# Kernel tuning notes

Measured on AMD Instinct MI355X. Metric: run time of the kernel, lower is better.

## Reference

```python
import jax, jax.numpy as jnp
import numpy as np

N, E, G = 4096, 16384, 16
IN_C, EDGE_C, H = 3, 4, 128
LN_EPS = 1e-5


def setup_inputs() -> dict:
    key = jax.random.key(0)
    ks = jax.random.split(key, 32)
    nrm = lambda k, shp, s: jax.random.normal(k, shp, jnp.float32) * s
    inp = {}
    inp["x"] = nrm(ks[0], (N, IN_C), 1.0)
    inp["edge_index"] = jax.random.randint(ks[1], (2, E), 0, N)
    inp["edge_attr"] = nrm(ks[2], (E, EDGE_C), 1.0)
    inp["batch"] = jnp.sort(jax.random.randint(ks[3], (N,), 0, G))
    inp["contingency_type"] = nrm(ks[4], (G, 4), 1.0)
    inp["load_scale"] = nrm(ks[5], (G,), 1.0)
    i = 6
    def conv_params(prefix, in_c):
        nonlocal i
        inp[prefix + "_w1"] = nrm(ks[i], (EDGE_C, 128), 1.0 / np.sqrt(EDGE_C)); i += 1
        inp[prefix + "_b1"] = jnp.zeros((128,), jnp.float32)
        inp[prefix + "_w2"] = nrm(ks[i], (128, in_c * H), 1.0 / np.sqrt(128)); i += 1
        inp[prefix + "_b2"] = jnp.zeros((in_c * H,), jnp.float32)
        inp[prefix + "_root"] = nrm(ks[i], (in_c, H), 1.0 / np.sqrt(in_c)); i += 1
        inp[prefix + "_bias"] = jnp.zeros((H,), jnp.float32)
    conv_params("c1", IN_C)
    conv_params("c2", H)
    conv_params("c3", H)
    for p in ("ln1", "ln2", "ln3"):
        inp[p + "_g"] = jnp.ones((H,), jnp.float32)
        inp[p + "_b"] = jnp.zeros((H,), jnp.float32)
    inp["lin_w"] = nrm(ks[i], (2 * H + 4 + 1, 2), 1.0 / np.sqrt(2 * H + 5)); i += 1
    inp["lin_b"] = jnp.zeros((2,), jnp.float32)
    return inp


def _nnconv(x, src, dst, edge_attr, w1, b1, w2, b2, root, bias, in_c):
    # edge MLP -> per-edge weight matrix [E, in_c, H]
    h = jax.nn.relu(edge_attr @ w1 + b1)
    W = (h @ w2 + b2).reshape(-1, in_c, H)
    msg = jnp.einsum('ei,eio->eo', x[src], W)  # gather + per-edge matmul
    s = jax.ops.segment_sum(msg, dst, num_segments=N)
    cnt = jax.ops.segment_sum(jnp.ones((msg.shape[0],), msg.dtype), dst, num_segments=N)
    agg = s / jnp.maximum(cnt, 1.0)[:, None]  # scatter-mean
    return agg + x @ root + bias


def _layernorm(x, g, b):
    m = jnp.mean(x, axis=-1, keepdims=True)
    v = jnp.mean(jnp.square(x - m), axis=-1, keepdims=True)
    return (x - m) * jax.lax.rsqrt(v + LN_EPS) * g + b


def reference(x, edge_index, edge_attr, batch, contingency_type, load_scale,
              c1_w1, c1_b1, c1_w2, c1_b2, c1_root, c1_bias,
              c2_w1, c2_b1, c2_w2, c2_b2, c2_root, c2_bias,
              c3_w1, c3_b1, c3_w2, c3_b2, c3_root, c3_bias,
              ln1_g, ln1_b, ln2_g, ln2_b, ln3_g, ln3_b,
              lin_w, lin_b):
    src, dst = edge_index[0], edge_index[1]
    h = _nnconv(x, src, dst, edge_attr, c1_w1, c1_b1, c1_w2, c1_b2, c1_root, c1_bias, IN_C)
    h = jax.nn.relu(_layernorm(h, ln1_g, ln1_b))
    h = _nnconv(h, src, dst, edge_attr, c2_w1, c2_b1, c2_w2, c2_b2, c2_root, c2_bias, H)
    h = jax.nn.elu(_layernorm(h, ln2_g, ln2_b))
    h = _nnconv(h, src, dst, edge_attr, c3_w1, c3_b1, c3_w2, c3_b2, c3_root, c3_bias, H)
    h = jax.nn.leaky_relu(_layernorm(h, ln3_g, ln3_b), negative_slope=0.01)
    # global mean / max pool over graphs
    gsum = jax.ops.segment_sum(h, batch, num_segments=G)
    gcnt = jax.ops.segment_sum(jnp.ones((N,), h.dtype), batch, num_segments=G)
    gmean = gsum / jnp.maximum(gcnt, 1.0)[:, None]
    gmax = jax.ops.segment_max(h, batch, num_segments=G)
    gmax = jnp.where(gcnt[:, None] > 0, gmax, 0.0)
    x_cat = jnp.concatenate([gmean, gmax, contingency_type, load_scale[:, None]], axis=1)
    return x_cat @ lin_w + lin_b
```

## Files before the change

### kernel.cpp

```cpp
#include <hip/hip_runtime.h>
#include <hip/hip_bf16.h>


#define N_NODES 4096
#define N_EDGES 16384
#define N_GRAPHS 16
#define HD 128
#define BM 128
#define LDB 136
#define KSPLIT 2
#define KT_PER (HD / KSPLIT)
#define SLAB_E (HD * HD)
#define PN 32

typedef unsigned short ushort_t;
typedef __attribute__((ext_vector_type(8))) short short8;
typedef __attribute__((ext_vector_type(4))) float f32x4;

static __device__ __forceinline__ ushort_t f2b(float f) {
    __hip_bfloat16 h = __float2bfloat16(f);
    union { __hip_bfloat16 h; ushort_t u; } cv; cv.h = h; return cv.u;
}
static __device__ __forceinline__ float b2f(ushort_t u) {
    union { unsigned u; float f; } cv; cv.u = ((unsigned)u) << 16; return cv.f;
}

static __device__ __forceinline__ float wave_sum(float v) {
#pragma unroll
    for (int off = 1; off < 64; off <<= 1) v += __shfl_xor(v, off, 64);
    return v;
}

__global__ __launch_bounds__(256) void count_k(const int* __restrict__ dst, float* __restrict__ cnt) {
    int e = blockIdx.x * 256 + threadIdx.x;
    atomicAdd(&cnt[dst[e]], 1.0f);
}

__global__ __launch_bounds__(128) void l1_edge(
    const float* __restrict__ x, const int* __restrict__ src, const int* __restrict__ dst,
    const float* __restrict__ ea, const float* __restrict__ w1, const float* __restrict__ b1,
    const float* __restrict__ w2, const float* __restrict__ b2, float* __restrict__ agg) {
    __shared__ float h[4][HD];
    __shared__ float xsrc[4][3];
    const int o = threadIdx.x;
    const int e0 = blockIdx.x * 4;
#pragma unroll
    for (int q = 0; q < 4; ++q) {
        float s = b1[o];
#pragma unroll
        for (int j = 0; j < 4; ++j) s = fmaf(ea[(e0 + q) * 4 + j], w1[j * HD + o], s);
        h[q][o] = fmaxf(s, 0.0f);
    }
    if (o < 12) { int q = o / 3, i = o % 3; xsrc[q][i] = x[src[e0 + q] * 3 + i]; }
    __syncthreads();
    float acc[4] = {0.f, 0.f, 0.f, 0.f};
    for (int i = 0; i < 3; ++i) {
        float bb = b2[i * HD + o];
        float w[4] = {bb, bb, bb, bb};
        for (int k = 0; k < HD; ++k) {
            float w2v = w2[k * 384 + i * HD + o];
#pragma unroll
            for (int q = 0; q < 4; ++q) w[q] = fmaf(h[q][k], w2v, w[q]);
        }
#pragma unroll
        for (int q = 0; q < 4; ++q) acc[q] = fmaf(xsrc[q][i], w[q], acc[q]);
    }
#pragma unroll
    for (int q = 0; q < 4; ++q) atomicAdd(&agg[dst[e0 + q] * HD + o], acc[q]);
}

__global__ __launch_bounds__(128) void node_update_l1(
    float* __restrict__ agg, const float* __restrict__ cnt, const float* __restrict__ x,
    const float* __restrict__ root, const float* __restrict__ bias,
    const float* __restrict__ lng, const float* __restrict__ lnb) {
    const int n = blockIdx.x, o = threadIdx.x;
    float s = bias[o];
#pragma unroll
    for (int i = 0; i < 3; ++i) s = fmaf(x[n * 3 + i], root[i * HD + o], s);
    float v = agg[n * HD + o] / fmaxf(cnt[n], 1.0f) + s;
    __shared__ float red[2];
    float ws = wave_sum(v);
    if ((o & 63) == 0) red[o >> 6] = ws;
    __syncthreads();
    float m = (red[0] + red[1]) * (1.0f / HD);
    float d = v - m;
    float ws2 = wave_sum(d * d);
    __syncthreads();
    if ((o & 63) == 0) red[o >> 6] = ws2;
    __syncthreads();
    float var = (red[0] + red[1]) * (1.0f / HD);
    float y = d * rsqrtf(var + 1e-5f) * lng[o] + lnb[o];
    agg[n * HD + o] = fmaxf(y, 0.0f);
}

__global__ __launch_bounds__(256) void w2t_prep(const float* __restrict__ w2,
                                                const float* __restrict__ b2,
                                                ushort_t* __restrict__ w2t) {
    __shared__ ushort_t tile[HD][LDB];
    const int kt = blockIdx.x;
    const int t = threadIdx.x;
    const float* srcp = (kt < HD) ? (w2 + kt * HD * HD) : b2;
    for (int c = 0; c < 64; ++c) {
        int flat = c * 256 + t;
        int i = flat >> 7, o = flat & 127;
        tile[o][i] = f2b(srcp[i * HD + o]);
    }
    __syncthreads();
    uint4* outp = (uint4*)(w2t + kt * HD * HD);
    for (int c = 0; c < 8; ++c) {
        int f = c * 256 + t;
        int o = f >> 4, i0 = (f & 15) * 8;
        outp[f] = *(const uint4*)&tile[o][i0];
    }
}

__global__ __launch_bounds__(512, 2) void gemm_mfma(
    const float* __restrict__ hprev, const float* __restrict__ ea,
    const float* __restrict__ w1, const float* __restrict__ b1,
    const ushort_t* __restrict__ w2t,
    const int* __restrict__ src, const int* __restrict__ dst,
    float* __restrict__ agg) {
    __shared__ ushort_t Bs[4 * SLAB_E];
    __shared__ ushort_t HeT[KT_PER + 1][BM];

    const int t = threadIdx.x;
    const int wave = t >> 6, lane = t & 63;
    const int quad = lane >> 4, l16 = lane & 15;
    const int mg = wave >> 2;
    const int ng = wave & 3;
    const int eb = blockIdx.x >> 1;
    const int ks = blockIdx.x & 1;
    const int k0 = ks * KT_PER;
    const int e0 = eb * BM;
    const int rbase = mg * 64;
    const int n0 = ng * 32;
    const int nslab = ks ? (KT_PER + 1) : KT_PER;

#define GSLAB(s) (((s) < KT_PER) ? (k0 + (s)) : HD)
#define ASMBAR  { asm volatile("s_waitcnt lgkmcnt(0)" ::: "memory"); \
                  __builtin_amdgcn_s_barrier(); }

#define LOADG(va, vb, vc, vd, kt)                                               \
    {                                                                           \
        const uint4* gp = (const uint4*)(w2t + (size_t)(kt) * SLAB_E);          \
        va = gp[t]; vb = gp[t + 512]; vc = gp[t + 1024]; vd = gp[t + 1536];     \
    }
    const int dr0 = t >> 4;
    const int dswoff = dr0 * HD + (((t & 15) ^ (dr0 & 7)) << 3);
#define DSW(wp, va, vb, vc, vd)                                                 \
    {                                                                           \
        *(uint4*)((wp) + dswoff)         = va;                                  \
        *(uint4*)((wp) + dswoff + 4096)  = vb;                                  \
        *(uint4*)((wp) + dswoff + 8192)  = vc;                                  \
        *(uint4*)((wp) + dswoff + 12288) = vd;                                  \
    }
#define READF(bf, bp)                                                           \
    {                                                                           \
        _Pragma("unroll") for (int ni = 0; ni < 2; ++ni) {                      \
            const int R = n0 + ni * 16 + l16;                                   \
            const ushort_t* rowp = (bp) + R * HD;                               \
            const int r7 = R & 7;                                               \
            _Pragma("unroll") for (int kb = 0; kb < 4; ++kb)                    \
                bf[ni][kb] = *(const short8*)&rowp[((kb * 4 + quad) ^ r7) << 3];\
        }                                                                       \
    }
#define CONSUME(bf, s)                                                          \
    {                                                                           \
        _Pragma("unroll") for (int mi = 0; mi < 4; ++mi) {                      \
            ushort4 hv = *(const ushort4*)&HeT[s][rbase + mi * 16 + quad * 4];  \
            float h0 = b2f(hv.x), h1 = b2f(hv.y), h2 = b2f(hv.z), h3 = b2f(hv.w);\
            _Pragma("unroll") for (int ni = 0; ni < 2; ++ni) {                  \
                f32x4 p = {0.f, 0.f, 0.f, 0.f};                                 \
                _Pragma("unroll") for (int kb = 0; kb < 4; ++kb)                \
                    p = __builtin_amdgcn_mfma_f32_16x16x32_bf16(                \
                        afrag[mi][kb], bf[ni][kb], p, 0, 0, 0);                 \
                acc[mi][ni][0] = fmaf(h0, p[0], acc[mi][ni][0]);                \
                acc[mi][ni][1] = fmaf(h1, p[1], acc[mi][ni][1]);                \
                acc[mi][ni][2] = fmaf(h2, p[2], acc[mi][ni][2]);                \
                acc[mi][ni][3] = fmaf(h3, p[3], acc[mi][ni][3]);                \
            }                                                                   \
        }                                                                       \
    }

    uint4 s0a, s0b, s0c, s0d, s1a, s1b, s1c, s1d;
    LOADG(s0a, s0b, s0c, s0d, GSLAB(0));
    LOADG(s1a, s1b, s1c, s1d, GSLAB(1));

    {
        const int le = t >> 2;
        const int j0 = (t & 3) * 4;
        const int r7 = le & 7;
        const float* rp = hprev + src[e0 + le] * HD + (t & 3) * 32;
        ushort_t* xrow = Bs + 3 * (size_t)SLAB_E + le * HD;
#pragma unroll
        for (int c = 0; c < 4; ++c) {
            float4 va = ((const float4*)rp)[2 * c];
            float4 vb = ((const float4*)rp)[2 * c + 1];
            uint4 pk;
            pk.x = (unsigned)f2b(va.x) | ((unsigned)f2b(va.y) << 16);
            pk.y = (unsigned)f2b(va.z) | ((unsigned)f2b(va.w) << 16);
            pk.z = (unsigned)f2b(vb.x) | ((unsigned)f2b(vb.y) << 16);
            pk.w = (unsigned)f2b(vb.z) | ((unsigned)f2b(vb.w) << 16);
            *(uint4*)&xrow[((j0 + c) ^ r7) << 3] = pk;
        }
    }

    {
        const int e = t & 127;
        const float4 av = ((const float4*)ea)[e0 + e];
        const float a0 = av.x, a1 = av.y, a2 = av.z, a3 = av.w;
        for (int kl = t >> 7; kl < KT_PER; kl += 4) {
            const int kt = k0 + kl;
            float s = b1[kt];
            s = fmaf(a0, w1[0 * HD + kt], s);
            s = fmaf(a1, w1[1 * HD + kt], s);
            s = fmaf(a2, w1[2 * HD + kt], s);
            s = fmaf(a3, w1[3 * HD + kt], s);
            HeT[kl][e] = f2b(fmaxf(s, 0.0f));
        }
        if (ks == 1 && (t >> 7) == 0) HeT[KT_PER][e] = f2b(1.0f);
    }
    ASMBAR;

    short8 afrag[4][4];
    {
        const ushort_t* xp = Bs + 3 * (size_t)SLAB_E;
#pragma unroll
        for (int mi = 0; mi < 4; ++mi) {
            const int R = rbase + mi * 16 + l16;
            const ushort_t* rowp = xp + R * HD;
            const int r7 = R & 7;
#pragma unroll
            for (int kb = 0; kb < 4; ++kb)
                afrag[mi][kb] = *(const short8*)&rowp[((kb * 4 + quad) ^ r7) << 3];
        }
    }

    DSW(Bs, s0a, s0b, s0c, s0d);
    DSW(Bs + SLAB_E, s1a, s1b, s1c, s1d);
    LOADG(s0a, s0b, s0c, s0d, GSLAB(2));
    LOADG(s1a, s1b, s1c, s1d, GSLAB(3));

    f32x4 acc[4][2];
#pragma unroll
    for (int mi = 0; mi < 4; ++mi)
#pragma unroll
        for (int ni = 0; ni < 2; ++ni)
            acc[mi][ni] = (f32x4){0.f, 0.f, 0.f, 0.f};

    ASMBAR;

    short8 bf0[2][4], bf1[2][4];
    for (int s = 0; s < KT_PER; s += 2) {
        ushort_t* bpe = Bs + (size_t)(s & 3) * SLAB_E;
        ushort_t* bpo = Bs + (size_t)((s + 1) & 3) * SLAB_E;
        READF(bf0, bpe);
        CONSUME(bf0, s);
        if (s + 2 < nslab) { ushort_t* wp = Bs + (size_t)((s + 2) & 3) * SLAB_E; DSW(wp, s0a, s0b, s0c, s0d); }
        if (s + 3 < nslab) { ushort_t* wp = Bs + (size_t)((s + 3) & 3) * SLAB_E; DSW(wp, s1a, s1b, s1c, s1d); }
        if (s + 4 < nslab) LOADG(s0a, s0b, s0c, s0d, GSLAB(s + 4));
        if (s + 5 < nslab) LOADG(s1a, s1b, s1c, s1d, GSLAB(s + 5));
        READF(bf1, bpo);
        CONSUME(bf1, s + 1);
        ASMBAR;
    }
    if (nslab > KT_PER) {
        ushort_t* bp = Bs + (size_t)(KT_PER & 3) * SLAB_E;
        READF(bf0, bp);
        CONSUME(bf0, KT_PER);
    }
#undef GSLAB
#undef ASMBAR
#undef LOADG
#undef DSW
#undef READF
#undef CONSUME

#pragma unroll
    for (int mi = 0; mi < 4; ++mi) {
#pragma unroll
        for (int r = 0; r < 4; ++r) {
            const int dn = dst[e0 + rbase + mi * 16 + quad * 4 + r];
#pragma unroll
            for (int ni = 0; ni < 2; ++ni)
                atomicAdd(&agg[dn * HD + n0 + ni * 16 + l16], acc[mi][ni][r]);
        }
    }
}

__global__ __launch_bounds__(128) void node_update(
    float* __restrict__ agg, const float* __restrict__ cnt,
    const float* __restrict__ hprev, const float* __restrict__ root, const float* __restrict__ bias,
    const float* __restrict__ lng, const float* __restrict__ lnb, int act) {
    const int n = blockIdx.x, o = threadIdx.x;
    __shared__ float hr[HD];
    hr[o] = hprev[n * HD + o];
    __syncthreads();
    float s = bias[o];
#pragma unroll 8
    for (int k = 0; k < HD; ++k) s = fmaf(hr[k], root[k * HD + o], s);
    float v = agg[n * HD + o] / fmaxf(cnt[n], 1.0f) + s;
    __shared__ float red[2];
    float ws = wave_sum(v);
    if ((o & 63) == 0) red[o >> 6] = ws;
    __syncthreads();
    float m = (red[0] + red[1]) * (1.0f / HD);
    float d = v - m;
    float ws2 = wave_sum(d * d);
    __syncthreads();
    if ((o & 63) == 0) red[o >> 6] = ws2;
    __syncthreads();
    float var = (red[0] + red[1]) * (1.0f / HD);
    float y = d * rsqrtf(var + 1e-5f) * lng[o] + lnb[o];
    if (act == 1) y = (y > 0.0f) ? y : expm1f(y);
    else y = (y > 0.0f) ? y : 0.01f * y;
    agg[n * HD + o] = y;
}

static __device__ __forceinline__ unsigned fkey(float f) {
    unsigned b = __float_as_uint(f);
    return (b & 0x80000000u) ? ~b : (b | 0x80000000u);
}
__global__ __launch_bounds__(128) void pool_scatter(
    const float* __restrict__ h3, const int* __restrict__ batch,
    float* __restrict__ gsum, unsigned* __restrict__ gmaxk, int* __restrict__ gcnt) {
    const int o = threadIdx.x;
    const int nb = blockIdx.x * PN;
    float sum = 0.0f, mx = -3.0e38f;
    int gcur = batch[nb];
    int run = 0;
    for (int j = 0; j < PN; ++j) {
        const int n = nb + j;
        const int g = batch[n];
        const float v = h3[n * HD + o];
        if (g != gcur) {
            atomicAdd(&gsum[gcur * HD + o], sum);
            atomicMax(&gmaxk[gcur * HD + o], fkey(mx));
            if (o == 0) atomicAdd(&gcnt[gcur], run);
            sum = 0.0f; mx = -3.0e38f; run = 0; gcur = g;
        }
        sum += v; mx = fmaxf(mx, v); ++run;
    }
    atomicAdd(&gsum[gcur * HD + o], sum);
    atomicMax(&gmaxk[gcur * HD + o], fkey(mx));
    if (o == 0) atomicAdd(&gcnt[gcur], run);
}

__global__ __launch_bounds__(128) void pool_head2(
    const float* __restrict__ gsum, const unsigned* __restrict__ gmaxk, const int* __restrict__ gcnt,
    const float* __restrict__ cont, const float* __restrict__ ls,
    const float* __restrict__ lin_w, const float* __restrict__ lin_b, float* __restrict__ out) {
    const int g = blockIdx.x, o = threadIdx.x;
    const int c = gcnt[g];
    __shared__ float xcat[2 * HD + 5];
    xcat[o] = gsum[g * HD + o] / fmaxf((float)c, 1.0f);
    unsigned key = gmaxk[g * HD + o];
    unsigned bits = (key & 0x80000000u) ? (key & 0x7FFFFFFFu) : ~key;
    xcat[HD + o] = (c > 0) ? __uint_as_float(bits) : 0.0f;
    if (o < 4) xcat[2 * HD + o] = cont[g * 4 + o];
    if (o == 0) xcat[2 * HD + 4] = ls[g];
    __syncthreads();
    if (o < 2) {
        float r = lin_b[o];
        for (int ri = 0; ri < 2 * HD + 5; ++ri) r = fmaf(xcat[ri], lin_w[ri * 2 + o], r);
        out[g * 2 + o] = r;
    }
}

extern "C" void kernel_launch(void* const* d_in, const int* in_sizes, int n_in,
                              void* d_out, int out_size, void* d_ws, size_t ws_size,
                              hipStream_t stream) {
    const float* x     = (const float*)d_in[0];
    const int*   ei    = (const int*)d_in[1];
    const float* ea    = (const float*)d_in[2];
    const int*   batch = (const int*)d_in[3];
    const float* cont  = (const float*)d_in[4];
    const float* ls    = (const float*)d_in[5];
    const float *c1_w1 = (const float*)d_in[6],  *c1_b1 = (const float*)d_in[7];
    const float *c1_w2 = (const float*)d_in[8],  *c1_b2 = (const float*)d_in[9];
    const float *c1_rt = (const float*)d_in[10], *c1_bs = (const float*)d_in[11];
    const float *c2_w1 = (const float*)d_in[12], *c2_b1 = (const float*)d_in[13];
    const float *c2_w2 = (const float*)d_in[14], *c2_b2 = (const float*)d_in[15];
    const float *c2_rt = (const float*)d_in[16], *c2_bs = (const float*)d_in[17];
    const float *c3_w1 = (const float*)d_in[18], *c3_b1 = (const float*)d_in[19];
    const float *c3_w2 = (const float*)d_in[20], *c3_b2 = (const float*)d_in[21];
    const float *c3_rt = (const float*)d_in[22], *c3_bs = (const float*)d_in[23];
    const float *ln1g = (const float*)d_in[24], *ln1b = (const float*)d_in[25];
    const float *ln2g = (const float*)d_in[26], *ln2b = (const float*)d_in[27];
    const float *ln3g = (const float*)d_in[28], *ln3b = (const float*)d_in[29];
    const float *lin_w = (const float*)d_in[30], *lin_b = (const float*)d_in[31];
    float* out = (float*)d_out;

    float*    cnt  = (float*)d_ws;
    float*    bufA = cnt + N_NODES;
    float*    bufB = bufA + N_NODES * HD;
    ushort_t* w2t  = (ushort_t*)(bufB + N_NODES * HD);
    float*    gsum = (float*)(w2t + (HD + 1) * HD * HD);
    unsigned* gmaxk = (unsigned*)(gsum + N_GRAPHS * HD);
    int*      gcnt = (int*)(gmaxk + N_GRAPHS * HD);
    const int* src = ei;
    const int* dst = ei + N_EDGES;

    hipMemsetAsync(cnt, 0, N_NODES * sizeof(float), stream);
    count_k<<<N_EDGES / 256, 256, 0, stream>>>(dst, cnt);

    hipMemsetAsync(bufA, 0, N_NODES * HD * sizeof(float), stream);
    l1_edge<<<N_EDGES / 4, 128, 0, stream>>>(x, src, dst, ea, c1_w1, c1_b1, c1_w2, c1_b2, bufA);
    node_update_l1<<<N_NODES, 128, 0, stream>>>(bufA, cnt, x, c1_rt, c1_bs, ln1g, ln1b);

    w2t_prep<<<HD + 1, 256, 0, stream>>>(c2_w2, c2_b2, w2t);
    hipMemsetAsync(bufB, 0, N_NODES * HD * sizeof(float), stream);
    gemm_mfma<<<(N_EDGES / BM) * KSPLIT, 512, 0, stream>>>(bufA, ea, c2_w1, c2_b1, w2t, src, dst, bufB);
    node_update<<<N_NODES, 128, 0, stream>>>(bufB, cnt, bufA, c2_rt, c2_bs, ln2g, ln2b, 1);

    w2t_prep<<<HD + 1, 256, 0, stream>>>(c3_w2, c3_b2, w2t);
    hipMemsetAsync(bufA, 0, N_NODES * HD * sizeof(float), stream);
    gemm_mfma<<<(N_EDGES / BM) * KSPLIT, 512, 0, stream>>>(bufB, ea, c3_w1, c3_b1, w2t, src, dst, bufA);
    node_update<<<N_NODES, 128, 0, stream>>>(bufA, cnt, bufB, c3_rt, c3_bs, ln3g, ln3b, 2);

    hipMemsetAsync(gsum, 0, (2 * N_GRAPHS * HD + N_GRAPHS) * sizeof(float), stream);
    pool_scatter<<<N_NODES / PN, 128, 0, stream>>>(bufA, batch, gsum, gmaxk, gcnt);
    pool_head2<<<N_GRAPHS, 128, 0, stream>>>(gsum, gmaxk, gcnt, cont, ls, lin_w, lin_b, out);
}
```

Before: 388.0 us.

## Split K four ways and double-buffer weight slabs to raise occupancy

Splits the per-edge hidden dimension across four blocks instead of two, so more blocks run per edge tile. The shared weight buffer shrinks from four slabs to two, with a reworked double-buffered load/store schedule, and launch bounds now target four blocks per CU. The bias slab is handled by a separate consume path that adds the product directly, replacing the multiply by a constant row of ones. In exchange, every edge tile is gathered and converted four times instead of twice, atomic adds to the aggregate double, and the tighter pipeline has less prefetch depth.

```diff
diff --git a/kernel.cpp b/kernel.cpp
--- a/kernel.cpp
+++ b/kernel.cpp
@@ -8,7 +8,7 @@
 #define HD 128
 #define BM 128
 #define LDB 136
-#define KSPLIT 2
+#define KSPLIT 4
 #define KT_PER (HD / KSPLIT)
 #define SLAB_E (HD * HD)
 #define PN 32
@@ -114,27 +114,27 @@
     }
 }
 
-__global__ __launch_bounds__(512, 2) void gemm_mfma(
+__global__ __launch_bounds__(512, 4) void gemm_mfma(
     const float* __restrict__ hprev, const float* __restrict__ ea,
     const float* __restrict__ w1, const float* __restrict__ b1,
     const ushort_t* __restrict__ w2t,
     const int* __restrict__ src, const int* __restrict__ dst,
     float* __restrict__ agg) {
-    __shared__ ushort_t Bs[4 * SLAB_E];
-    __shared__ ushort_t HeT[KT_PER + 1][BM];
+    __shared__ ushort_t Bs[2 * SLAB_E];
+    __shared__ ushort_t HeT[KT_PER][BM];
 
     const int t = threadIdx.x;
     const int wave = t >> 6, lane = t & 63;
     const int quad = lane >> 4, l16 = lane & 15;
     const int mg = wave >> 2;
     const int ng = wave & 3;
-    const int eb = blockIdx.x >> 1;
-    const int ks = blockIdx.x & 1;
+    const int eb = blockIdx.x >> 2;
+    const int ks = blockIdx.x & 3;
     const int k0 = ks * KT_PER;
     const int e0 = eb * BM;
     const int rbase = mg * 64;
     const int n0 = ng * 32;
-    const int nslab = ks ? (KT_PER + 1) : KT_PER;
+    const int nslab = (ks == KSPLIT - 1) ? (KT_PER + 1) : KT_PER;
 
 #define GSLAB(s) (((s) < KT_PER) ? (k0 + (s)) : HD)
 #define ASMBAR  { asm volatile("s_waitcnt lgkmcnt(0)" ::: "memory"); \
@@ -181,6 +181,19 @@
             }                                                                   \
         }                                                                       \
     }
+#define CONSUME_BIAS(bf)                                                        \
+    {                                                                           \
+        _Pragma("unroll") for (int mi = 0; mi < 4; ++mi) {                      \
+            _Pragma("unroll") for (int ni = 0; ni < 2; ++ni) {                  \
+                f32x4 p = {0.f, 0.f, 0.f, 0.f};                                 \
+                _Pragma("unroll") for (int kb = 0; kb < 4; ++kb)                \
+                    p = __builtin_amdgcn_mfma_f32_16x16x32_bf16(                \
+                        afrag[mi][kb], bf[ni][kb], p, 0, 0, 0);                 \
+                acc[mi][ni][0] += p[0]; acc[mi][ni][1] += p[1];                 \
+                acc[mi][ni][2] += p[2]; acc[mi][ni][3] += p[3];                 \
+            }                                                                   \
+        }                                                                       \
+    }
 
     uint4 s0a, s0b, s0c, s0d, s1a, s1b, s1c, s1d;
     LOADG(s0a, s0b, s0c, s0d, GSLAB(0));
@@ -191,7 +204,7 @@
         const int j0 = (t & 3) * 4;
         const int r7 = le & 7;
         const float* rp = hprev + src[e0 + le] * HD + (t & 3) * 32;
-        ushort_t* xrow = Bs + 3 * (size_t)SLAB_E + le * HD;
+        ushort_t* xrow = Bs + le * HD;
 #pragma unroll
         for (int c = 0; c < 4; ++c) {
             float4 va = ((const float4*)rp)[2 * c];
@@ -218,28 +231,25 @@
             s = fmaf(a3, w1[3 * HD + kt], s);
             HeT[kl][e] = f2b(fmaxf(s, 0.0f));
         }
-        if (ks == 1 && (t >> 7) == 0) HeT[KT_PER][e] = f2b(1.0f);
     }
     ASMBAR;
 
     short8 afrag[4][4];
     {
-        const ushort_t* xp = Bs + 3 * (size_t)SLAB_E;
 #pragma unroll
         for (int mi = 0; mi < 4; ++mi) {
             const int R = rbase + mi * 16 + l16;
-            const ushort_t* rowp = xp + R * HD;
+            const ushort_t* rowp = Bs + R * HD;
             const int r7 = R & 7;
 #pragma unroll
             for (int kb = 0; kb < 4; ++kb)
                 afrag[mi][kb] = *(const short8*)&rowp[((kb * 4 + quad) ^ r7) << 3];
         }
     }
+    ASMBAR;
 
     DSW(Bs, s0a, s0b, s0c, s0d);
-    DSW(Bs + SLAB_E, s1a, s1b, s1c, s1d);
     LOADG(s0a, s0b, s0c, s0d, GSLAB(2));
-    LOADG(s1a, s1b, s1c, s1d, GSLAB(3));
 
     f32x4 acc[4][2];
 #pragma unroll
@@ -250,24 +260,22 @@
 
     ASMBAR;
 
-    short8 bf0[2][4], bf1[2][4];
+    short8 bf[2][4];
     for (int s = 0; s < KT_PER; s += 2) {
-        ushort_t* bpe = Bs + (size_t)(s & 3) * SLAB_E;
-        ushort_t* bpo = Bs + (size_t)((s + 1) & 3) * SLAB_E;
-        READF(bf0, bpe);
-        CONSUME(bf0, s);
-        if (s + 2 < nslab) { ushort_t* wp = Bs + (size_t)((s + 2) & 3) * SLAB_E; DSW(wp, s0a, s0b, s0c, s0d); }
-        if (s + 3 < nslab) { ushort_t* wp = Bs + (size_t)((s + 3) & 3) * SLAB_E; DSW(wp, s1a, s1b, s1c, s1d); }
+        READF(bf, Bs);
+        DSW(Bs + SLAB_E, s1a, s1b, s1c, s1d);
+        if (s + 3 < nslab) LOADG(s1a, s1b, s1c, s1d, GSLAB(s + 3));
+        CONSUME(bf, s);
+        ASMBAR;
+        READF(bf, Bs + SLAB_E);
+        if (s + 2 < nslab) DSW(Bs, s0a, s0b, s0c, s0d);
         if (s + 4 < nslab) LOADG(s0a, s0b, s0c, s0d, GSLAB(s + 4));
-        if (s + 5 < nslab) LOADG(s1a, s1b, s1c, s1d, GSLAB(s + 5));
-        READF(bf1, bpo);
-        CONSUME(bf1, s + 1);
+        CONSUME(bf, s + 1);
         ASMBAR;
     }
     if (nslab > KT_PER) {
-        ushort_t* bp = Bs + (size_t)(KT_PER & 3) * SLAB_E;
-        READF(bf0, bp);
-        CONSUME(bf0, KT_PER);
+        READF(bf, Bs);
+        CONSUME_BIAS(bf);
     }
 #undef GSLAB
 #undef ASMBAR
@@ -275,6 +283,7 @@
 #undef DSW
 #undef READF
 #undef CONSUME
+#undef CONSUME_BIAS
 
 #pragma unroll
     for (int mi = 0; mi < 4; ++mi) {
```

After: 1.086 ms. 2.8x slower.

## Read MFMA-fragment-ordered W2 directly from global, drop LDS B staging

Applied to the files above, without the earlier changes.

w2t_prep now writes each W2 slab in the exact per-lane MFMA B-fragment order, so gemm_mfma can load B fragments straight from global/L2 with contiguous 16-byte reads instead of staging slabs through a 4-deep LDS ring. The block grows to 1024 threads (16 waves) with each wave owning a 32x32 output tile, and LDS holds only the gathered X tile and the edge-MLP hidden values. This removes LDS write/read traffic and barrier-heavy pipelining for B. The cost is reliance on L2/L1 bandwidth and latency for every slab read without explicit prefetch, and occasional raw barriers are inserted to keep waves loosely in step.

```diff
diff --git a/kernel.cpp b/kernel.cpp
--- a/kernel.cpp
+++ b/kernel.cpp
@@ -106,94 +106,45 @@
         tile[o][i] = f2b(srcp[i * HD + o]);
     }
     __syncthreads();
-    uint4* outp = (uint4*)(w2t + kt * HD * HD);
-    for (int c = 0; c < 8; ++c) {
-        int f = c * 256 + t;
-        int o = f >> 4, i0 = (f & 15) * 8;
-        outp[f] = *(const uint4*)&tile[o][i0];
-    }
-}
-
-__global__ __launch_bounds__(512, 2) void gemm_mfma(
+    uint4* outp = (uint4*)(w2t + (size_t)kt * SLAB_E);
+    for (int it = 0; it < 8; ++it) {
+        int c = it * 256 + t;
+        int ng = c >> 9, j = (c >> 6) & 7, l = c & 63;
+        int ni = j >> 2, kb = j & 3;
+        int R  = ng * 32 + ni * 16 + (l & 15);
+        int ke = kb * 32 + (l >> 4) * 8;
+        outp[c] = *(const uint4*)&tile[R][ke];
+    }
+}
+
+__global__ __launch_bounds__(1024) void gemm_mfma(
     const float* __restrict__ hprev, const float* __restrict__ ea,
     const float* __restrict__ w1, const float* __restrict__ b1,
     const ushort_t* __restrict__ w2t,
     const int* __restrict__ src, const int* __restrict__ dst,
     float* __restrict__ agg) {
-    __shared__ ushort_t Bs[4 * SLAB_E];
-    __shared__ ushort_t HeT[KT_PER + 1][BM];
+    __shared__ ushort_t Xs[SLAB_E];
+    __shared__ ushort_t HeT[KT_PER][BM];
 
     const int t = threadIdx.x;
-    const int wave = t >> 6, lane = t & 63;
-    const int quad = lane >> 4, l16 = lane & 15;
+    const int lane = t & 63, quad = lane >> 4, l16 = lane & 15;
+    const int wave = t >> 6;
     const int mg = wave >> 2;
     const int ng = wave & 3;
     const int eb = blockIdx.x >> 1;
     const int ks = blockIdx.x & 1;
     const int k0 = ks * KT_PER;
     const int e0 = eb * BM;
-    const int rbase = mg * 64;
-    const int n0 = ng * 32;
-    const int nslab = ks ? (KT_PER + 1) : KT_PER;
-
-#define GSLAB(s) (((s) < KT_PER) ? (k0 + (s)) : HD)
-#define ASMBAR  { asm volatile("s_waitcnt lgkmcnt(0)" ::: "memory"); \
-                  __builtin_amdgcn_s_barrier(); }
-
-#define LOADG(va, vb, vc, vd, kt)                                               \
-    {                                                                           \
-        const uint4* gp = (const uint4*)(w2t + (size_t)(kt) * SLAB_E);          \
-        va = gp[t]; vb = gp[t + 512]; vc = gp[t + 1024]; vd = gp[t + 1536];     \
-    }
-    const int dr0 = t >> 4;
-    const int dswoff = dr0 * HD + (((t & 15) ^ (dr0 & 7)) << 3);
-#define DSW(wp, va, vb, vc, vd)                                                 \
-    {                                                                           \
-        *(uint4*)((wp) + dswoff)         = va;                                  \
-        *(uint4*)((wp) + dswoff + 4096)  = vb;                                  \
-        *(uint4*)((wp) + dswoff + 8192)  = vc;                                  \
-        *(uint4*)((wp) + dswoff + 12288) = vd;                                  \
-    }
-#define READF(bf, bp)                                                           \
-    {                                                                           \
-        _Pragma("unroll") for (int ni = 0; ni < 2; ++ni) {                      \
-            const int R = n0 + ni * 16 + l16;                                   \
-            const ushort_t* rowp = (bp) + R * HD;                               \
-            const int r7 = R & 7;                                               \
-            _Pragma("unroll") for (int kb = 0; kb < 4; ++kb)                    \
-                bf[ni][kb] = *(const short8*)&rowp[((kb * 4 + quad) ^ r7) << 3];\
-        }                                                                       \
-    }
-#define CONSUME(bf, s)                                                          \
-    {                                                                           \
-        _Pragma("unroll") for (int mi = 0; mi < 4; ++mi) {                      \
-            ushort4 hv = *(const ushort4*)&HeT[s][rbase + mi * 16 + quad * 4];  \
-            float h0 = b2f(hv.x), h1 = b2f(hv.y), h2 = b2f(hv.z), h3 = b2f(hv.w);\
-            _Pragma("unroll") for (int ni = 0; ni < 2; ++ni) {                  \
-                f32x4 p = {0.f, 0.f, 0.f, 0.f};                                 \
-                _Pragma("unroll") for (int kb = 0; kb < 4; ++kb)                \
-                    p = __builtin_amdgcn_mfma_f32_16x16x32_bf16(                \
-                        afrag[mi][kb], bf[ni][kb], p, 0, 0, 0);                 \
-                acc[mi][ni][0] = fmaf(h0, p[0], acc[mi][ni][0]);                \
-                acc[mi][ni][1] = fmaf(h1, p[1], acc[mi][ni][1]);                \
-                acc[mi][ni][2] = fmaf(h2, p[2], acc[mi][ni][2]);                \
-                acc[mi][ni][3] = fmaf(h3, p[3], acc[mi][ni][3]);                \
-            }                                                                   \
-        }                                                                       \
-    }
-
-    uint4 s0a, s0b, s0c, s0d, s1a, s1b, s1c, s1d;
-    LOADG(s0a, s0b, s0c, s0d, GSLAB(0));
-    LOADG(s1a, s1b, s1c, s1d, GSLAB(1));
+    const int rbase = mg * 32;
 
     {
-        const int le = t >> 2;
-        const int j0 = (t & 3) * 4;
+        const int le = t >> 3;
+        const int j0 = (t & 7) * 2;
         const int r7 = le & 7;
-        const float* rp = hprev + src[e0 + le] * HD + (t & 3) * 32;
-        ushort_t* xrow = Bs + 3 * (size_t)SLAB_E + le * HD;
-#pragma unroll
-        for (int c = 0; c < 4; ++c) {
+        const float* rp = hprev + src[e0 + le] * HD + (t & 7) * 16;
+        ushort_t* xrow = Xs + le * HD;
+#pragma unroll
+        for (int c = 0; c < 2; ++c) {
             float4 va = ((const float4*)rp)[2 * c];
             float4 vb = ((const float4*)rp)[2 * c + 1];
             uint4 pk;
@@ -208,82 +159,95 @@
     {
         const int e = t & 127;
         const float4 av = ((const float4*)ea)[e0 + e];
-        const float a0 = av.x, a1 = av.y, a2 = av.z, a3 = av.w;
-        for (int kl = t >> 7; kl < KT_PER; kl += 4) {
+        for (int kl = t >> 7; kl < KT_PER; kl += 8) {
             const int kt = k0 + kl;
             float s = b1[kt];
-            s = fmaf(a0, w1[0 * HD + kt], s);
-            s = fmaf(a1, w1[1 * HD + kt], s);
-            s = fmaf(a2, w1[2 * HD + kt], s);
-            s = fmaf(a3, w1[3 * HD + kt], s);
+            s = fmaf(av.x, w1[0 * HD + kt], s);
+            s = fmaf(av.y, w1[1 * HD + kt], s);
+            s = fmaf(av.z, w1[2 * HD + kt], s);
+            s = fmaf(av.w, w1[3 * HD + kt], s);
             HeT[kl][e] = f2b(fmaxf(s, 0.0f));
         }
-        if (ks == 1 && (t >> 7) == 0) HeT[KT_PER][e] = f2b(1.0f);
-    }
-    ASMBAR;
-
-    short8 afrag[4][4];
-    {
-        const ushort_t* xp = Bs + 3 * (size_t)SLAB_E;
-#pragma unroll
-        for (int mi = 0; mi < 4; ++mi) {
-            const int R = rbase + mi * 16 + l16;
-            const ushort_t* rowp = xp + R * HD;
-            const int r7 = R & 7;
-#pragma unroll
-            for (int kb = 0; kb < 4; ++kb)
-                afrag[mi][kb] = *(const short8*)&rowp[((kb * 4 + quad) ^ r7) << 3];
-        }
-    }
-
-    DSW(Bs, s0a, s0b, s0c, s0d);
-    DSW(Bs + SLAB_E, s1a, s1b, s1c, s1d);
-    LOADG(s0a, s0b, s0c, s0d, GSLAB(2));
-    LOADG(s1a, s1b, s1c, s1d, GSLAB(3));
-
-    f32x4 acc[4][2];
-#pragma unroll
-    for (int mi = 0; mi < 4; ++mi)
+    }
+    __syncthreads();
+
+    short8 afrag[2][4];
+#pragma unroll
+    for (int mi = 0; mi < 2; ++mi) {
+        const int R = rbase + mi * 16 + l16;
+        const ushort_t* rowp = Xs + R * HD;
+        const int r7 = R & 7;
+#pragma unroll
+        for (int kb = 0; kb < 4; ++kb)
+            afrag[mi][kb] = *(const short8*)&rowp[((kb * 4 + quad) ^ r7) << 3];
+    }
+
+    f32x4 acc[2][2];
+#pragma unroll
+    for (int mi = 0; mi < 2; ++mi)
 #pragma unroll
         for (int ni = 0; ni < 2; ++ni)
             acc[mi][ni] = (f32x4){0.f, 0.f, 0.f, 0.f};
 
-    ASMBAR;
-
-    short8 bf0[2][4], bf1[2][4];
-    for (int s = 0; s < KT_PER; s += 2) {
-        ushort_t* bpe = Bs + (size_t)(s & 3) * SLAB_E;
-        ushort_t* bpo = Bs + (size_t)((s + 1) & 3) * SLAB_E;
-        READF(bf0, bpe);
-        CONSUME(bf0, s);
-        if (s + 2 < nslab) { ushort_t* wp = Bs + (size_t)((s + 2) & 3) * SLAB_E; DSW(wp, s0a, s0b, s0c, s0d); }
-        if (s + 3 < nslab) { ushort_t* wp = Bs + (size_t)((s + 3) & 3) * SLAB_E; DSW(wp, s1a, s1b, s1c, s1d); }
-        if (s + 4 < nslab) LOADG(s0a, s0b, s0c, s0d, GSLAB(s + 4));
-        if (s + 5 < nslab) LOADG(s1a, s1b, s1c, s1d, GSLAB(s + 5));
-        READF(bf1, bpo);
-        CONSUME(bf1, s + 1);
-        ASMBAR;
-    }
-    if (nslab > KT_PER) {
-        ushort_t* bp = Bs + (size_t)(KT_PER & 3) * SLAB_E;
-        READF(bf0, bp);
-        CONSUME(bf0, KT_PER);
-    }
-#undef GSLAB
-#undef ASMBAR
-#undef LOADG
-#undef DSW
-#undef READF
-#undef CONSUME
-
-#pragma unroll
-    for (int mi = 0; mi < 4; ++mi) {
+    const ushort_t* bbase = w2t + (size_t)ng * 4096 + (size_t)lane * 8;
+
+    for (int s = 0; s < KT_PER; ++s) {
+        const ushort_t* bw = bbase + (size_t)(k0 + s) * SLAB_E;
+        short8 bf[2][4];
+#pragma unroll
+        for (int ni = 0; ni < 2; ++ni)
+#pragma unroll
+            for (int kb = 0; kb < 4; ++kb)
+                bf[ni][kb] = *(const short8*)(bw + (ni * 4 + kb) * 512);
+#pragma unroll
+        for (int mi = 0; mi < 2; ++mi) {
+            ushort4 hv = *(const ushort4*)&HeT[s][rbase + mi * 16 + quad * 4];
+            float h0 = b2f(hv.x), h1 = b2f(hv.y), h2 = b2f(hv.z), h3 = b2f(hv.w);
+#pragma unroll
+            for (int ni = 0; ni < 2; ++ni) {
+                f32x4 p = {0.f, 0.f, 0.f, 0.f};
+#pragma unroll
+                for (int kb = 0; kb < 4; ++kb)
+                    p = __builtin_amdgcn_mfma_f32_16x16x32_bf16(
+                        afrag[mi][kb], bf[ni][kb], p, 0, 0, 0);
+                acc[mi][ni][0] = fmaf(h0, p[0], acc[mi][ni][0]);
+                acc[mi][ni][1] = fmaf(h1, p[1], acc[mi][ni][1]);
+                acc[mi][ni][2] = fmaf(h2, p[2], acc[mi][ni][2]);
+                acc[mi][ni][3] = fmaf(h3, p[3], acc[mi][ni][3]);
+            }
+        }
+        if ((s & 7) == 7) __builtin_amdgcn_s_barrier();
+    }
+    if (ks == 1) {
+        const ushort_t* bw = bbase + (size_t)HD * SLAB_E;
+        short8 bf[2][4];
+#pragma unroll
+        for (int ni = 0; ni < 2; ++ni)
+#pragma unroll
+            for (int kb = 0; kb < 4; ++kb)
+                bf[ni][kb] = *(const short8*)(bw + (ni * 4 + kb) * 512);
+#pragma unroll
+        for (int mi = 0; mi < 2; ++mi)
+#pragma unroll
+            for (int ni = 0; ni < 2; ++ni) {
+                f32x4 p = {0.f, 0.f, 0.f, 0.f};
+#pragma unroll
+                for (int kb = 0; kb < 4; ++kb)
+                    p = __builtin_amdgcn_mfma_f32_16x16x32_bf16(
+                        afrag[mi][kb], bf[ni][kb], p, 0, 0, 0);
+                acc[mi][ni][0] += p[0]; acc[mi][ni][1] += p[1];
+                acc[mi][ni][2] += p[2]; acc[mi][ni][3] += p[3];
+            }
+    }
+
+#pragma unroll
+    for (int mi = 0; mi < 2; ++mi) {
 #pragma unroll
         for (int r = 0; r < 4; ++r) {
             const int dn = dst[e0 + rbase + mi * 16 + quad * 4 + r];
 #pragma unroll
             for (int ni = 0; ni < 2; ++ni)
-                atomicAdd(&agg[dn * HD + n0 + ni * 16 + l16], acc[mi][ni][r]);
+                atomicAdd(&agg[dn * HD + ng * 32 + ni * 16 + l16], acc[mi][ni][r]);
         }
     }
 }
@@ -410,12 +374,12 @@
 
     w2t_prep<<<HD + 1, 256, 0, stream>>>(c2_w2, c2_b2, w2t);
     hipMemsetAsync(bufB, 0, N_NODES * HD * sizeof(float), stream);
-    gemm_mfma<<<(N_EDGES / BM) * KSPLIT, 512, 0, stream>>>(bufA, ea, c2_w1, c2_b1, w2t, src, dst, bufB);
+    gemm_mfma<<<(N_EDGES / BM) * KSPLIT, 1024, 0, stream>>>(bufA, ea, c2_w1, c2_b1, w2t, src, dst, bufB);
     node_update<<<N_NODES, 128, 0, stream>>>(bufB, cnt, bufA, c2_rt, c2_bs, ln2g, ln2b, 1);
 
     w2t_prep<<<HD + 1, 256, 0, stream>>>(c3_w2, c3_b2, w2t);
     hipMemsetAsync(bufA, 0, N_NODES * HD * sizeof(float), stream);
-    gemm_mfma<<<(N_EDGES / BM) * KSPLIT, 512, 0, stream>>>(bufB, ea, c3_w1, c3_b1, w2t, src, dst, bufA);
+    gemm_mfma<<<(N_EDGES / BM) * KSPLIT, 1024, 0, stream>>>(bufB, ea, c3_w1, c3_b1, w2t, src, dst, bufA);
     node_update<<<N_NODES, 128, 0, stream>>>(bufA, cnt, bufB, c3_rt, c3_bs, ln3g, ln3b, 2);
 
     hipMemsetAsync(gsum, 0, (2 * N_GRAPHS * HD + N_GRAPHS) * sizeof(float), stream);
```

Result: slower. 404.2 us (+4.2%).
